# Kernel optimization log

Hardware: AMD Instinct MI355X
Metric: run time of the kernel (lower is better)

The kernel has to match this reference:

```python
import jax, jax.numpy as jnp
import numpy as np

LOG2 = np.float32(np.log(2.0))

def _jsd_pos(p):
    # get_positive_expectation, measure='JSD', average=False
    return LOG2 - jax.nn.softplus(-p)

def setup_inputs() -> dict:
    key = jax.random.key(0)
    k1, k2, k3, k4, k5, k6 = jax.random.split(key, 6)
    N, G, D = 65536, 512, 256
    batch_1 = jnp.sort(jax.random.randint(k1, (N,), 0, G))
    batch_2 = jnp.sort(jax.random.randint(k2, (N,), 0, G))
    z1 = jax.random.normal(k3, (N, D), dtype=jnp.float32)
    z2 = jax.random.normal(k4, (N, D), dtype=jnp.float32)
    g1 = jax.random.normal(k5, (G, D), dtype=jnp.float32)
    g2 = jax.random.normal(k6, (G, D), dtype=jnp.float32)
    return {"batch_1": batch_1, "batch_2": batch_2, "z1": z1, "z2": z2, "g1": g1, "g2": g2}

def reference(batch_1, batch_2, z1, z2, g1, g2):
    # pos_mask scatter-build -> dense one-hot [N, G]
    pos_mask_1 = jax.nn.one_hot(batch_1, g1.shape[0], dtype=z1.dtype)
    pos_mask_2 = jax.nn.one_hot(batch_2, g2.shape[0], dtype=z2.dtype)
    # masked node-graph similarity matrices [N, G]
    self_sim_1 = (z1 @ g1.T) * pos_mask_1
    self_sim_2 = (z2 @ g2.T) * pos_mask_2
    cross_sim_12 = (z1 @ g2.T) * pos_mask_1
    cross_sim_21 = (z2 @ g1.T) * pos_mask_2
    # sep=True branch: per-node row sums, L2 distance over nodes
    self_js_11 = _jsd_pos(self_sim_1).sum(1)
    cross_js_12 = _jsd_pos(cross_sim_12).sum(1)
    self_js_22 = _jsd_pos(self_sim_2).sum(1)
    cross_js_21 = _jsd_pos(cross_sim_21).sum(1)
    L_1 = jnp.sqrt(jnp.sum((self_js_11 - cross_js_12) ** 2))
    L_2 = jnp.sqrt(jnp.sum((self_js_22 - cross_js_21) ** 2))
    return L_1 + L_2
```

## Files before the change

### kernel.cpp

```cpp
#include <hip/hip_runtime.h>
#include <math.h>

__device__ __forceinline__ float spn(float p) {
    return fmaxf(-p, 0.0f) + __logf(1.0f + __expf(-fabsf(p)));
}

__device__ __forceinline__ float dot4(float4 a, float4 b) {
    return a.x * b.x + a.y * b.y + a.z * b.z + a.w * b.w;
}

__device__ __forceinline__ float wave64_reduce(float x) {
    int t;
    t = __builtin_amdgcn_update_dpp(0, __builtin_bit_cast(int, x), 0x111, 0xf, 0xf, true);
    x += __builtin_bit_cast(float, t);
    t = __builtin_amdgcn_update_dpp(0, __builtin_bit_cast(int, x), 0x112, 0xf, 0xf, true);
    x += __builtin_bit_cast(float, t);
    t = __builtin_amdgcn_update_dpp(0, __builtin_bit_cast(int, x), 0x114, 0xf, 0xf, true);
    x += __builtin_bit_cast(float, t);
    t = __builtin_amdgcn_update_dpp(0, __builtin_bit_cast(int, x), 0x118, 0xf, 0xf, true);
    x += __builtin_bit_cast(float, t);
    t = __builtin_amdgcn_update_dpp(0, __builtin_bit_cast(int, x), 0x142, 0xa, 0xf, true);
    x += __builtin_bit_cast(float, t);
    t = __builtin_amdgcn_update_dpp(0, __builtin_bit_cast(int, x), 0x143, 0xc, 0xf, true);
    x += __builtin_bit_cast(float, t);
    return x;
}

#define NBLOCKS 4096
#define WAVES_PER_BLOCK 8
#define NODES_PER_WAVE 2

__global__ __launch_bounds__(512) void jsd_dot_kernel(
    const int*   __restrict__ b1,
    const int*   __restrict__ b2,
    const float* __restrict__ z1,
    const float* __restrict__ z2,
    const float* __restrict__ g1,
    const float* __restrict__ g2,
    float*       __restrict__ partials)
{
    const int wave = threadIdx.x >> 6;
    const int lane = threadIdx.x & 63;
    const int w    = blockIdx.x * WAVES_PER_BLOCK + wave;
    const int base = w * NODES_PER_WAVE;

    const int sbase = __builtin_amdgcn_readfirstlane(base);

    const int i1_0 = b1[sbase + 0];
    const int i1_1 = b1[sbase + 1];
    const int i2_0 = b2[sbase + 0];
    const int i2_1 = b2[sbase + 1];

    const float4* z1p = (const float4*)(z1 + (size_t)sbase * 256);
    const float4* z2p = (const float4*)(z2 + (size_t)sbase * 256);

    const float4 a1_0  = z1p[lane];
    const float4 a2_0  = z2p[lane];
    const float4 a1_1  = z1p[64 + lane];
    const float4 a2_1  = z2p[64 + lane];
    const float4 w11_0 = ((const float4*)(g1 + (size_t)i1_0 * 256))[lane];
    const float4 w12_0 = ((const float4*)(g2 + (size_t)i1_0 * 256))[lane];
    const float4 w22_0 = ((const float4*)(g2 + (size_t)i2_0 * 256))[lane];
    const float4 w21_0 = ((const float4*)(g1 + (size_t)i2_0 * 256))[lane];
    const float4 w11_1 = ((const float4*)(g1 + (size_t)i1_1 * 256))[lane];
    const float4 w12_1 = ((const float4*)(g2 + (size_t)i1_1 * 256))[lane];
    const float4 w22_1 = ((const float4*)(g2 + (size_t)i2_1 * 256))[lane];
    const float4 w21_1 = ((const float4*)(g1 + (size_t)i2_1 * 256))[lane];

    __builtin_amdgcn_sched_barrier(0);

    float acc1 = 0.0f, acc2 = 0.0f;

    {
        float s11 = wave64_reduce(dot4(a1_0, w11_0));
        float c12 = wave64_reduce(dot4(a1_0, w12_0));
        float s22 = wave64_reduce(dot4(a2_0, w22_0));
        float c21 = wave64_reduce(dot4(a2_0, w21_0));
        if (lane == 63) {
            float d1 = spn(c12) - spn(s11);
            float d2 = spn(c21) - spn(s22);
            acc1 += d1 * d1;
            acc2 += d2 * d2;
        }
    }
    {
        float s11 = wave64_reduce(dot4(a1_1, w11_1));
        float c12 = wave64_reduce(dot4(a1_1, w12_1));
        float s22 = wave64_reduce(dot4(a2_1, w22_1));
        float c21 = wave64_reduce(dot4(a2_1, w21_1));
        if (lane == 63) {
            float d1 = spn(c12) - spn(s11);
            float d2 = spn(c21) - spn(s22);
            acc1 += d1 * d1;
            acc2 += d2 * d2;
        }
    }

    __shared__ float s1[WAVES_PER_BLOCK], s2[WAVES_PER_BLOCK];
    if (lane == 63) { s1[wave] = acc1; s2[wave] = acc2; }
    __syncthreads();

    if (threadIdx.x == 0) {
        float t1 = 0.0f, t2 = 0.0f;
        #pragma unroll
        for (int k = 0; k < WAVES_PER_BLOCK; ++k) { t1 += s1[k]; t2 += s2[k]; }
        partials[blockIdx.x * 2 + 0] = t1;
        partials[blockIdx.x * 2 + 1] = t2;
    }
}

__global__ __launch_bounds__(256) void jsd_reduce_kernel(
    const float* __restrict__ partials,
    float*       __restrict__ out)
{
    const int tid  = threadIdx.x;
    const int wave = tid >> 6;
    const int lane = tid & 63;

    float a = 0.0f, b = 0.0f;
    #pragma unroll
    for (int i = 0; i < NBLOCKS / 256; ++i) {
        a += partials[(i * 256 + tid) * 2 + 0];
        b += partials[(i * 256 + tid) * 2 + 1];
    }

    a = wave64_reduce(a);
    b = wave64_reduce(b);

    __shared__ float s1[4], s2[4];
    if (lane == 63) { s1[wave] = a; s2[wave] = b; }
    __syncthreads();

    if (tid == 0) {
        float t1 = s1[0] + s1[1] + s1[2] + s1[3];
        float t2 = s2[0] + s2[1] + s2[2] + s2[3];
        out[0] = sqrtf(t1) + sqrtf(t2);
    }
}

extern "C" void kernel_launch(void* const* d_in, const int* in_sizes, int n_in,
                              void* d_out, int out_size, void* d_ws, size_t ws_size,
                              hipStream_t stream) {
    const int*   b1 = (const int*)  d_in[0];
    const int*   b2 = (const int*)  d_in[1];
    const float* z1 = (const float*)d_in[2];
    const float* z2 = (const float*)d_in[3];
    const float* g1 = (const float*)d_in[4];
    const float* g2 = (const float*)d_in[5];
    float* out      = (float*)d_out;
    float* partials = (float*)d_ws;

    jsd_dot_kernel<<<NBLOCKS, 512, 0, stream>>>(b1, b2, z1, z2, g1, g2, partials);
    jsd_reduce_kernel<<<1, 256, 0, stream>>>(partials, out);
}
```

Measured before the change: 153.6 us.

## Stage z and g rows into LDS via global_load_lds with two rounds per wave

Replaces direct register loads of the z and gathered g rows with asynchronous global-to-LDS loads (global_load_lds, 16 bytes per lane) into a per-wave LDS slice. Each wave then reads the rows back from LDS for the dot products. Blocks shrink to 4 waves and each wave handles two rounds of two nodes, so the grid size stays the same. The aim is to cut VGPR pressure and issue more loads in flight. The cost is 48KB of LDS per block, which limits occupancy, plus a full vmcnt wait per round that serializes the rounds.

After: 158.4 us. +3.1%, slower.

```diff
diff --git a/kernel.cpp b/kernel.cpp
--- a/kernel.cpp
+++ b/kernel.cpp
@@ -1,5 +1,10 @@
 #include <hip/hip_runtime.h>
 #include <math.h>
+
+#define D 256
+#define NBLOCKS 4096
+#define WAVES 4
+#define ROUNDS 2
 
 __device__ __forceinline__ float spn(float p) {
     return fmaxf(-p, 0.0f) + __logf(1.0f + __expf(-fabsf(p)));
@@ -26,11 +31,14 @@
     return x;
 }
 
-#define NBLOCKS 4096
-#define WAVES_PER_BLOCK 8
-#define NODES_PER_WAVE 2
+__device__ __forceinline__ void stage_row(const float* grow, float* ldsrow, int lane) {
+    __builtin_amdgcn_global_load_lds(
+        (const __attribute__((address_space(1))) void*)((const float4*)grow + lane),
+        (__attribute__((address_space(3))) void*)ldsrow,
+        16, 0, 0);
+}
 
-__global__ __launch_bounds__(512) void jsd_dot_kernel(
+__global__ __launch_bounds__(256) void jsd_dot_stage_kernel(
     const int*   __restrict__ b1,
     const int*   __restrict__ b2,
     const float* __restrict__ z1,
@@ -39,71 +47,92 @@
     const float* __restrict__ g2,
     float*       __restrict__ partials)
 {
+    __shared__ float lds[WAVES * 12 * D];
+    __shared__ float s1[WAVES], s2[WAVES];
+
     const int wave = threadIdx.x >> 6;
     const int lane = threadIdx.x & 63;
-    const int w    = blockIdx.x * WAVES_PER_BLOCK + wave;
-    const int base = w * NODES_PER_WAVE;
+    float* const slice = lds + wave * 12 * D;
 
-    const int sbase = __builtin_amdgcn_readfirstlane(base);
-
-    const int i1_0 = b1[sbase + 0];
-    const int i1_1 = b1[sbase + 1];
-    const int i2_0 = b2[sbase + 0];
-    const int i2_1 = b2[sbase + 1];
-
-    const float4* z1p = (const float4*)(z1 + (size_t)sbase * 256);
-    const float4* z2p = (const float4*)(z2 + (size_t)sbase * 256);
-
-    const float4 a1_0  = z1p[lane];
-    const float4 a2_0  = z2p[lane];
-    const float4 a1_1  = z1p[64 + lane];
-    const float4 a2_1  = z2p[64 + lane];
-    const float4 w11_0 = ((const float4*)(g1 + (size_t)i1_0 * 256))[lane];
-    const float4 w12_0 = ((const float4*)(g2 + (size_t)i1_0 * 256))[lane];
-    const float4 w22_0 = ((const float4*)(g2 + (size_t)i2_0 * 256))[lane];
-    const float4 w21_0 = ((const float4*)(g1 + (size_t)i2_0 * 256))[lane];
-    const float4 w11_1 = ((const float4*)(g1 + (size_t)i1_1 * 256))[lane];
-    const float4 w12_1 = ((const float4*)(g2 + (size_t)i1_1 * 256))[lane];
-    const float4 w22_1 = ((const float4*)(g2 + (size_t)i2_1 * 256))[lane];
-    const float4 w21_1 = ((const float4*)(g1 + (size_t)i2_1 * 256))[lane];
-
-    __builtin_amdgcn_sched_barrier(0);
+    const int nb0 = __builtin_amdgcn_readfirstlane(blockIdx.x * (WAVES * 2 * ROUNDS) + wave * 2);
 
     float acc1 = 0.0f, acc2 = 0.0f;
 
-    {
-        float s11 = wave64_reduce(dot4(a1_0, w11_0));
-        float c12 = wave64_reduce(dot4(a1_0, w12_0));
-        float s22 = wave64_reduce(dot4(a2_0, w22_0));
-        float c21 = wave64_reduce(dot4(a2_0, w21_0));
-        if (lane == 63) {
-            float d1 = spn(c12) - spn(s11);
-            float d2 = spn(c21) - spn(s22);
-            acc1 += d1 * d1;
-            acc2 += d2 * d2;
+    #pragma unroll
+    for (int r = 0; r < ROUNDS; ++r) {
+        const int n0 = nb0 + r * (WAVES * 2);
+        const int n1 = n0 + 1;
+
+        stage_row(z1 + (size_t)n0 * D, slice + 0 * D, lane);
+        stage_row(z2 + (size_t)n0 * D, slice + 1 * D, lane);
+        stage_row(z1 + (size_t)n1 * D, slice + 6 * D, lane);
+        stage_row(z2 + (size_t)n1 * D, slice + 7 * D, lane);
+
+        const int i1_0 = b1[n0];
+        const int i1_1 = b1[n1];
+        const int i2_0 = b2[n0];
+        const int i2_1 = b2[n1];
+
+        stage_row(g1 + (size_t)i1_0 * D, slice + 2 * D, lane);
+        stage_row(g2 + (size_t)i1_0 * D, slice + 3 * D, lane);
+        stage_row(g2 + (size_t)i2_0 * D, slice + 4 * D, lane);
+        stage_row(g1 + (size_t)i2_0 * D, slice + 5 * D, lane);
+        stage_row(g1 + (size_t)i1_1 * D, slice + 8 * D, lane);
+        stage_row(g2 + (size_t)i1_1 * D, slice + 9 * D, lane);
+        stage_row(g2 + (size_t)i2_1 * D, slice + 10 * D, lane);
+        stage_row(g1 + (size_t)i2_1 * D, slice + 11 * D, lane);
+
+        asm volatile("s_waitcnt vmcnt(0)" ::: "memory");
+        __builtin_amdgcn_sched_barrier(0);
+
+        {
+            const float4 a1  = ((const float4*)(slice + 0 * D))[lane];
+            const float4 a2  = ((const float4*)(slice + 1 * D))[lane];
+            const float4 w11 = ((const float4*)(slice + 2 * D))[lane];
+            const float4 w12 = ((const float4*)(slice + 3 * D))[lane];
+            const float4 w22 = ((const float4*)(slice + 4 * D))[lane];
+            const float4 w21 = ((const float4*)(slice + 5 * D))[lane];
+            float s11 = wave64_reduce(dot4(a1, w11));
+            float c12 = wave64_reduce(dot4(a1, w12));
+            float s22 = wave64_reduce(dot4(a2, w22));
+            float c21 = wave64_reduce(dot4(a2, w21));
+            if (lane == 63) {
+                float d1 = spn(c12) - spn(s11);
+                float d2 = spn(c21) - spn(s22);
+                acc1 += d1 * d1;
+                acc2 += d2 * d2;
+            }
         }
-    }
-    {
-        float s11 = wave64_reduce(dot4(a1_1, w11_1));
-        float c12 = wave64_reduce(dot4(a1_1, w12_1));
-        float s22 = wave64_reduce(dot4(a2_1, w22_1));
-        float c21 = wave64_reduce(dot4(a2_1, w21_1));
-        if (lane == 63) {
-            float d1 = spn(c12) - spn(s11);
-            float d2 = spn(c21) - spn(s22);
-            acc1 += d1 * d1;
-            acc2 += d2 * d2;
+        {
+            const float4 a1  = ((const float4*)(slice + 6 * D))[lane];
+            const float4 a2  = ((const float4*)(slice + 7 * D))[lane];
+            const float4 w11 = ((const float4*)(slice + 8 * D))[lane];
+            const float4 w12 = ((const float4*)(slice + 9 * D))[lane];
+            const float4 w22 = ((const float4*)(slice + 10 * D))[lane];
+            const float4 w21 = ((const float4*)(slice + 11 * D))[lane];
+            float s11 = wave64_reduce(dot4(a1, w11));
+            float c12 = wave64_reduce(dot4(a1, w12));
+            float s22 = wave64_reduce(dot4(a2, w22));
+            float c21 = wave64_reduce(dot4(a2, w21));
+            if (lane == 63) {
+                float d1 = spn(c12) - spn(s11);
+                float d2 = spn(c21) - spn(s22);
+                acc1 += d1 * d1;
+                acc2 += d2 * d2;
+            }
         }
+
+        asm volatile("s_waitcnt lgkmcnt(0)" ::: "memory");
+        __builtin_amdgcn_sched_barrier(0);
     }
 
-    __shared__ float s1[WAVES_PER_BLOCK], s2[WAVES_PER_BLOCK];
     if (lane == 63) { s1[wave] = acc1; s2[wave] = acc2; }
     __syncthreads();
 
     if (threadIdx.x == 0) {
         float t1 = 0.0f, t2 = 0.0f;
         #pragma unroll
-        for (int k = 0; k < WAVES_PER_BLOCK; ++k) { t1 += s1[k]; t2 += s2[k]; }
+        for (int k = 0; k < WAVES; ++k) { t1 += s1[k]; t2 += s2[k]; }
         partials[blockIdx.x * 2 + 0] = t1;
         partials[blockIdx.x * 2 + 1] = t2;
     }
@@ -150,6 +179,6 @@
     float* out      = (float*)d_out;
     float* partials = (float*)d_ws;
 
-    jsd_dot_kernel<<<NBLOCKS, 512, 0, stream>>>(b1, b2, z1, z2, g1, g2, partials);
+    jsd_dot_stage_kernel<<<NBLOCKS, 256, 0, stream>>>(b1, b2, z1, z2, g1, g2, partials);
     jsd_reduce_kernel<<<1, 256, 0, stream>>>(partials, out);
 }
```
